# Kernel optimization log

Measured on AMD Instinct MI355X. Metric: run time of the kernel, lower is better.

## Reference

```python
import jax, jax.numpy as jnp
import numpy as np

N0, N1, N2, N3 = 1_000_000, 300_000, 80_000, 30_000
CIN, C = 4, 64  # in_channels, INIT_DIM / PLANES[0]
K = 27          # 3x3x3 octree kernel
EPS = 1e-5      # BatchNorm eps


def octree_conv(x, neigh, W):
    """Octree sparse conv as gather + GEMM.
    x: [Nin, Cin], neigh: [Nout, K] int indices into x, W: [K, Cin, Cout].
    """
    g = x[neigh]                              # [Nout, K, Cin] irregular gather
    return jnp.einsum('nkc,kcd->nd', g, W)    # [Nout, Cout]


def batchnorm(x, gamma, beta):
    # BatchNorm1d in training mode: batch stats over node dim, biased variance
    m = jnp.mean(x, axis=0)
    v = jnp.var(x, axis=0)
    return (x - m) * jax.lax.rsqrt(v + EPS) * gamma + beta


def setup_inputs() -> dict:
    key = jax.random.key(0)
    ks = jax.random.split(key, 16)
    s = 0.05
    return {
        'x': jax.random.normal(ks[0], (N0, CIN), jnp.float32),
        'neigh_stem': jax.random.randint(ks[1], (N1, K), 0, N0, jnp.int32),
        'pool_child': jax.random.randint(ks[2], (N2, 8), 0, N1, jnp.int32),
        'neigh_ds': jax.random.randint(ks[3], (N3, K), 0, N2, jnp.int32),
        'neigh_res': jax.random.randint(ks[4], (N3, K), 0, N3, jnp.int32),
        'W_stem': jax.random.normal(ks[5], (K, CIN, C), jnp.float32) * s,
        'g_stem': jnp.ones((C,), jnp.float32),
        'b_stem': jnp.zeros((C,), jnp.float32),
        'W1': jax.random.normal(ks[6], (K, C, C), jnp.float32) * s,
        'g1': jnp.ones((C,), jnp.float32),
        'b1': jnp.zeros((C,), jnp.float32),
        'W2': jax.random.normal(ks[7], (K, C, C), jnp.float32) * s,
        'g2': jnp.ones((C,), jnp.float32),
        'b2': jnp.zeros((C,), jnp.float32),
        'Wd': jax.random.normal(ks[8], (K, C, C), jnp.float32) * s,
        'gd': jnp.ones((C,), jnp.float32),
        'bd': jnp.zeros((C,), jnp.float32),
    }


def reference(x, neigh_stem, pool_child, neigh_ds, neigh_res,
              W_stem, g_stem, b_stem, W1, g1, b1, W2, g2, b2, Wd, gd, bd):
    # StemLayer: conv(s2) -> BN -> ReLU -> OctreeMaxPool
    h = jax.nn.relu(batchnorm(octree_conv(x, neigh_stem, W_stem), g_stem, b_stem))  # [N1, C]
    h = jnp.max(h[pool_child], axis=1)                                              # [N2, C]
    # ResBlock stride=2 (layer1, blocks=1)
    out = jax.nn.relu(batchnorm(octree_conv(h, neigh_ds, W1), g1, b1))              # [N3, C]
    out = batchnorm(octree_conv(out, neigh_res, W2), g2, b2)                        # [N3, C]
    residual = batchnorm(octree_conv(h, neigh_ds, Wd), gd, bd)                      # DownSample shortcut
    return jax.nn.relu(out + residual)
```

## Files before the change

kernel.cpp:

```cpp
#include <hip/hip_runtime.h>

constexpr int CN0 = 1000000;
constexpr int CN1 = 300000;
constexpr int CN2 = 80000;
constexpr int CN3 = 30000;
constexpr float BN_EPS = 1e-5f;

typedef __attribute__((ext_vector_type(8))) short bf16x8;
typedef __attribute__((ext_vector_type(4))) float f32x4;

union FragU { uint4 u; bf16x8 b; };

__device__ __forceinline__ float2 bn_ab(float s, float q, float invn, float gamma, float beta) {
  float m = s * invn;
  float v = fmaf(q, invn, -m * m);
  float rstd = rsqrtf(v + BN_EPS);
  float a = gamma * rstd;
  float b = beta - m * a;
  return make_float2(a, b);
}

__device__ __forceinline__ unsigned short f2bf(float f) {
  unsigned u = __float_as_uint(f);
  u += 0x7FFFu + ((u >> 16) & 1u);
  return (unsigned short)(u >> 16);
}

__device__ __forceinline__ void sync_lds() {
  asm volatile("s_waitcnt lgkmcnt(0)" ::: "memory");
  __builtin_amdgcn_s_barrier();
  asm volatile("" ::: "memory");
}

__global__ __launch_bounds__(256) void k_prep_x(
    const float* __restrict__ x, unsigned int* __restrict__ xbf) {
  int i = blockIdx.x * 256 + threadIdx.x;
  if (i >= CN0) return;
  float4 v = *(const float4*)(x + i * 4);
  uint2 p;
  p.x = (unsigned)f2bf(v.x) | ((unsigned)f2bf(v.y) << 16);
  p.y = (unsigned)f2bf(v.z) | ((unsigned)f2bf(v.w) << 16);
  *(uint2*)(xbf + i * 2) = p;
}

__global__ __launch_bounds__(256) void k_prep_stem(
    const float* __restrict__ W, unsigned short* __restrict__ Wf) {
  int f = blockIdx.x * 256 + threadIdx.x;
  if (f >= 8192) return;
  int e = f & 7, lane = (f >> 3) & 63, nf = (f >> 9) & 3, ks = f >> 11;
  int k = ks * 32 + (lane >> 4) * 8 + e;
  int d = nf * 16 + (lane & 15);
  Wf[f] = (k < 108) ? f2bf(W[k * 64 + d]) : (unsigned short)0;
}

__global__ __launch_bounds__(256) void k_prep_dual(
    const float* __restrict__ W1, const float* __restrict__ Wd,
    unsigned short* __restrict__ Wdual) {
  int e = blockIdx.x * 256 + threadIdx.x;
  if (e >= 27 * 128 * 64) return;
  int cin = e & 63, d = (e >> 6) & 127, k = e >> 13;
  float v = (d < 64) ? W1[(k * 64 + cin) * 64 + d]
                     : Wd[(k * 64 + cin) * 64 + (d - 64)];
  Wdual[e] = f2bf(v);
}

__global__ __launch_bounds__(256) void k_prep_res(
    const float* __restrict__ W2, unsigned short* __restrict__ Wres) {
  int e = blockIdx.x * 256 + threadIdx.x;
  if (e >= 27 * 64 * 64) return;
  int cin = e & 63, d = (e >> 6) & 63, k = e >> 12;
  Wres[e] = f2bf(W2[(k * 64 + cin) * 64 + d]);
}

__global__ __launch_bounds__(256) void k_stem_mfma(
    const unsigned short* __restrict__ xbf, const int* __restrict__ neigh,
    const unsigned short* __restrict__ Wf, unsigned short* __restrict__ y1,
    float* __restrict__ stats) {
  constexpr int T = 4;
  __shared__ __align__(16) uint4 Bb[1024];
  const int tid = threadIdx.x;
  const int lane = tid & 63;
  const int wv = tid >> 6;
  const int l15 = lane & 15, lq = lane >> 4;
  const int g0 = blockIdx.x * T;

  {
    const uint4* Wsrc = (const uint4*)Wf;
#pragma unroll
    for (int j = 0; j < 4; ++j) Bb[tid + j * 256] = Wsrc[tid + j * 256];
  }
  __syncthreads();

  int idxA[8], idxB[8];
  FragU fragA[4], fragB[4];

#define LDIDX(g, dst)                                                   \
  {                                                                     \
    int node_ = (g)*64 + wv * 16 + l15;                                 \
    bool rowok_ = node_ < CN1;                                          \
    const int* nb_ = neigh + node_ * 27;                                \
    _Pragma("unroll") for (int ks_ = 0; ks_ < 4; ++ks_) {               \
      int tap0_ = ks_ * 8 + lq * 2;                                     \
      dst[ks_ * 2] = (rowok_ && tap0_ < 27) ? nb_[tap0_] : -1;          \
      dst[ks_ * 2 + 1] = (rowok_ && tap0_ + 1 < 27) ? nb_[tap0_ + 1] : -1; \
    }                                                                   \
  }

#define GATHER(idx, frag)                                               \
  {                                                                     \
    _Pragma("unroll") for (int ks_ = 0; ks_ < 4; ++ks_) {               \
      uint2 v0_ = {0u, 0u}, v1_ = {0u, 0u};                             \
      if (idx[ks_ * 2] >= 0)                                            \
        v0_ = *(const uint2*)(xbf + idx[ks_ * 2] * 4);                  \
      if (idx[ks_ * 2 + 1] >= 0)                                        \
        v1_ = *(const uint2*)(xbf + idx[ks_ * 2 + 1] * 4);              \
      frag[ks_].u.x = v0_.x; frag[ks_].u.y = v0_.y;                     \
      frag[ks_].u.z = v1_.x; frag[ks_].u.w = v1_.y;                     \
    }                                                                   \
  }

  LDIDX(g0 + 0, idxA);
  GATHER(idxA, fragA);
  LDIDX(g0 + 1, idxB);

  float sacc[4] = {0.f, 0.f, 0.f, 0.f};
  float qacc[4] = {0.f, 0.f, 0.f, 0.f};

#pragma unroll
  for (int t = 0; t < T; ++t) {
    FragU* cur = (t & 1) ? fragB : fragA;
    FragU* nxt = (t & 1) ? fragA : fragB;
    int* idn = (t & 1) ? idxA : idxB;
    int* idn2 = (t & 1) ? idxB : idxA;
    if (t + 1 < T) GATHER(idn, nxt);
    if (t + 2 < T) LDIDX(g0 + t + 2, idn2);

    f32x4 acc[4] = {};
#pragma unroll
    for (int ks = 0; ks < 4; ++ks) {
#pragma unroll
      for (int nf = 0; nf < 4; ++nf) {
        bf16x8 b = *(const bf16x8*)&Bb[(ks * 4 + nf) * 64 + lane];
        acc[nf] = __builtin_amdgcn_mfma_f32_16x16x32_bf16(cur[ks].b, b,
                                                          acc[nf], 0, 0, 0);
      }
    }

    int n0 = (g0 + t) * 64 + wv * 16;
#pragma unroll
    for (int nf = 0; nf < 4; ++nf) {
      int c = nf * 16 + l15;
#pragma unroll
      for (int r = 0; r < 4; ++r) {
        int row = n0 + lq * 4 + r;
        float v = acc[nf][r];
        if (row < CN1) y1[row * 64 + c] = f2bf(v);
        sacc[nf] += v;
        qacc[nf] = fmaf(v, v, qacc[nf]);
      }
    }
  }
#undef LDIDX
#undef GATHER

  __syncthreads();
  float* S = (float*)Bb;
#pragma unroll
  for (int nf = 0; nf < 4; ++nf) {
    float s = sacc[nf], q = qacc[nf];
    s += __shfl_xor(s, 16); s += __shfl_xor(s, 32);
    q += __shfl_xor(q, 16); q += __shfl_xor(q, 32);
    if (lane < 16) {
      S[wv * 64 + nf * 16 + lane] = s;
      S[256 + wv * 64 + nf * 16 + lane] = q;
    }
  }
  __syncthreads();
  if (tid < 64) {
    float s = S[tid] + S[64 + tid] + S[128 + tid] + S[192 + tid];
    float q = S[256 + tid] + S[320 + tid] + S[384 + tid] + S[448 + tid];
    atomicAdd(&stats[tid], s);
    atomicAdd(&stats[64 + tid], q);
  }
}

__global__ __launch_bounds__(256) void k_pool(
    const unsigned int* __restrict__ y1, const int* __restrict__ child,
    const float* __restrict__ stats, const float* __restrict__ gamma,
    const float* __restrict__ beta, unsigned int* __restrict__ h2) {
  const int tid = threadIdx.x;
  const int wd = tid & 31;
  const int n = blockIdx.x * 8 + (tid >> 5);
  const int c0 = wd * 2, c1 = c0 + 1;
  const int* crow = child + n * 8;
  int ch[8];
#pragma unroll
  for (int j = 0; j < 8; ++j) ch[j] = crow[j];
  unsigned vv[8];
#pragma unroll
  for (int j = 0; j < 8; ++j) vv[j] = y1[ch[j] * 32 + wd];

  float2 ab0 = bn_ab(stats[c0], stats[64 + c0], 1.0f / CN1, gamma[c0], beta[c0]);
  float2 ab1 = bn_ab(stats[c1], stats[64 + c1], 1.0f / CN1, gamma[c1], beta[c1]);
  float mx0 = -INFINITY, mn0 = INFINITY, mx1 = -INFINITY, mn1 = INFINITY;
#pragma unroll
  for (int j = 0; j < 8; ++j) {
    float v0 = __uint_as_float(vv[j] << 16);
    float v1 = __uint_as_float(vv[j] & 0xFFFF0000u);
    mx0 = fmaxf(mx0, v0); mn0 = fminf(mn0, v0);
    mx1 = fmaxf(mx1, v1); mn1 = fminf(mn1, v1);
  }
  float t0 = (ab0.x > 0.f) ? fmaf(ab0.x, mx0, ab0.y) : fmaf(ab0.x, mn0, ab0.y);
  float t1 = (ab1.x > 0.f) ? fmaf(ab1.x, mx1, ab1.y) : fmaf(ab1.x, mn1, ab1.y);
  unsigned o = (unsigned)f2bf(fmaxf(t0, 0.f)) |
               ((unsigned)f2bf(fmaxf(t1, 0.f)) << 16);
  h2[n * 32 + wd] = o;
}

template <int OUTC>
__global__ __launch_bounds__(256) void k_mconv(
    const unsigned short* __restrict__ src, const int* __restrict__ neigh,
    const unsigned short* __restrict__ Wblk, float* __restrict__ out,
    float* __restrict__ stats, int M) {
  constexpr int NF = OUTC / 32;
  constexpr int PPT = (OUTC * 128 / 16) / 256;
  __shared__ __align__(16) unsigned char Ab[64 * 128];
  __shared__ __align__(16) unsigned char Bb[OUTC * 128];
  __shared__ int nlds[64 * 27];

  const int tid = threadIdx.x;
  const int n0 = blockIdx.x * 64;
  const int lane = tid & 63;
  const int w = tid >> 6;
  const int wm = w >> 1, wn = w & 1;
  const int gi = tid >> 2;
  const int gq = tid & 3;
  const int swA = (gi & 7) << 4;

  for (int e = tid; e < 64 * 27; e += 256) {
    int row = n0 + e / 27;
    nlds[e] = (row < M) ? neigh[row * 27 + e % 27] : -1;
  }

  f32x4 acc[2][NF] = {};
  uint4 rA0 = {}, rA1 = {};
  uint4 rB[PPT];

  sync_lds();

  {
    int idx = nlds[gi * 27 + 0];
    if (idx >= 0) {
      const uint4* s = (const uint4*)(src + idx * 64 + gq * 16);
      rA0 = s[0]; rA1 = s[1];
    } else {
      rA0 = uint4{0, 0, 0, 0}; rA1 = uint4{0, 0, 0, 0};
    }
    const uint4* Bs = (const uint4*)(Wblk);
#pragma unroll
    for (int j = 0; j < PPT; ++j) rB[j] = Bs[tid * PPT + j];
  }

  for (int k = 0; k < 27; ++k) {
    *(uint4*)(Ab + gi * 128 + ((gq * 32) ^ swA)) = rA0;
    *(uint4*)(Ab + gi * 128 + ((gq * 32 + 16) ^ swA)) = rA1;
#pragma unroll
    for (int j = 0; j < PPT; ++j) {
      int p = tid * PPT + j;
      int d = p >> 3;
      int rb = (p & 7) * 16;
      *(uint4*)(Bb + d * 128 + (rb ^ ((d & 7) << 4))) = rB[j];
    }
    if (k < 26) {
      int idx = nlds[gi * 27 + k + 1];
      if (idx >= 0) {
        const uint4* s = (const uint4*)(src + idx * 64 + gq * 16);
        rA0 = s[0]; rA1 = s[1];
      } else {
        rA0 = uint4{0, 0, 0, 0}; rA1 = uint4{0, 0, 0, 0};
      }
      const uint4* Bs = (const uint4*)(Wblk + (k + 1) * OUTC * 64);
#pragma unroll
      for (int j = 0; j < PPT; ++j) rB[j] = Bs[tid * PPT + j];
    }
    sync_lds();
#pragma unroll
    for (int ks = 0; ks < 2; ++ks) {
      int kb = ks * 64 + (lane >> 4) * 16;
      bf16x8 a[2];
#pragma unroll
      for (int mf = 0; mf < 2; ++mf) {
        int r = wm * 32 + mf * 16 + (lane & 15);
        a[mf] = *(const bf16x8*)(Ab + r * 128 + (kb ^ ((r & 7) << 4)));
      }
#pragma unroll
      for (int nf = 0; nf < NF; ++nf) {
        int d = wn * (OUTC / 2) + nf * 16 + (lane & 15);
        bf16x8 b = *(const bf16x8*)(Bb + d * 128 + (kb ^ ((d & 7) << 4)));
#pragma unroll
        for (int mf = 0; mf < 2; ++mf)
          acc[mf][nf] = __builtin_amdgcn_mfma_f32_16x16x32_bf16(
              a[mf], b, acc[mf][nf], 0, 0, 0);
      }
    }
    sync_lds();
  }

#pragma unroll
  for (int mf = 0; mf < 2; ++mf) {
    int rbase = n0 + wm * 32 + mf * 16 + (lane >> 4) * 4;
#pragma unroll
    for (int nf = 0; nf < NF; ++nf) {
      int c = wn * (OUTC / 2) + nf * 16 + (lane & 15);
#pragma unroll
      for (int r = 0; r < 4; ++r) {
        int row = rbase + r;
        if (row < M) out[row * OUTC + c] = acc[mf][nf][r];
      }
    }
  }

#pragma unroll
  for (int nf = 0; nf < NF; ++nf) {
    float s = 0.f, q = 0.f;
#pragma unroll
    for (int mf = 0; mf < 2; ++mf)
#pragma unroll
      for (int r = 0; r < 4; ++r) {
        float v = acc[mf][nf][r];
        s += v; q += v * v;
      }
    s += __shfl_xor(s, 16); s += __shfl_xor(s, 32);
    q += __shfl_xor(q, 16); q += __shfl_xor(q, 32);
    if (lane < 16) {
      int c = wn * (OUTC / 2) + nf * 16 + lane;
      atomicAdd(&stats[c], s);
      atomicAdd(&stats[OUTC + c], q);
    }
  }
}

__global__ __launch_bounds__(256) void k_bnrelu(
    const float* __restrict__ y2d, const float* __restrict__ stats,
    const float* __restrict__ gamma, const float* __restrict__ beta,
    unsigned short* __restrict__ out1) {
  int e = blockIdx.x * 256 + threadIdx.x;
  int i = e >> 6, c = e & 63;
  float2 ab = bn_ab(stats[c], stats[128 + c], 1.0f / CN3, gamma[c], beta[c]);
  out1[e] = f2bf(fmaxf(fmaf(ab.x, y2d[i * 128 + c], ab.y), 0.f));
}

__global__ __launch_bounds__(256) void k_final(
    const float* __restrict__ y3, const float* __restrict__ y2d,
    const float* __restrict__ stats2, const float* __restrict__ stats1d,
    const float* __restrict__ g2, const float* __restrict__ b2,
    const float* __restrict__ gd, const float* __restrict__ bd,
    float* __restrict__ dout) {
  int e = blockIdx.x * 256 + threadIdx.x;
  int i = e >> 6, c = e & 63;
  float2 ab2 = bn_ab(stats2[c], stats2[64 + c], 1.0f / CN3, g2[c], b2[c]);
  float2 abd =
      bn_ab(stats1d[64 + c], stats1d[192 + c], 1.0f / CN3, gd[c], bd[c]);
  float o = fmaf(ab2.x, y3[e], ab2.y) + fmaf(abd.x, y2d[i * 128 + 64 + c], abd.y);
  dout[e] = fmaxf(o, 0.f);
}

extern "C" void kernel_launch(void* const* d_in, const int* in_sizes, int n_in,
                              void* d_out, int out_size, void* d_ws,
                              size_t ws_size, hipStream_t stream) {
  const float* x = (const float*)d_in[0];
  const int* neigh_stem = (const int*)d_in[1];
  const int* pool_child = (const int*)d_in[2];
  const int* neigh_ds = (const int*)d_in[3];
  const int* neigh_res = (const int*)d_in[4];
  const float* W_stem = (const float*)d_in[5];
  const float* g_stem = (const float*)d_in[6];
  const float* b_stem = (const float*)d_in[7];
  const float* W1 = (const float*)d_in[8];
  const float* g1 = (const float*)d_in[9];
  const float* b1 = (const float*)d_in[10];
  const float* W2 = (const float*)d_in[11];
  const float* g2 = (const float*)d_in[12];
  const float* b2 = (const float*)d_in[13];
  const float* Wd = (const float*)d_in[14];
  const float* gd = (const float*)d_in[15];
  const float* bd = (const float*)d_in[16];
  float* out = (float*)d_out;
  float* ws = (float*)d_ws;

  unsigned short* y1bf = (unsigned short*)ws;
  float* y2d = ws;
  unsigned short* out1bf = (unsigned short*)(ws + 3840000);
  float* y3 = ws + 4800000;
  unsigned short* h2bf = (unsigned short*)(ws + 9600000);
  unsigned int* xbf = (unsigned int*)(ws + 12160000);
  unsigned short* Wst = (unsigned short*)(ws + 14160000);
  unsigned short* Wdual = (unsigned short*)(ws + 14164096);
  unsigned short* Wres = (unsigned short*)(ws + 14274688);
  float* stats = ws + 14329984;
  float* stats_stem = stats;
  float* stats_1d = stats + 128;
  float* stats_2 = stats + 384;

  hipMemsetAsync(stats, 0, 512 * sizeof(float), stream);

  k_prep_x<<<(CN0 + 255) / 256, 256, 0, stream>>>(x, xbf);
  k_prep_stem<<<(8192 + 255) / 256, 256, 0, stream>>>(W_stem, Wst);
  k_prep_dual<<<(27 * 128 * 64 + 255) / 256, 256, 0, stream>>>(W1, Wd, Wdual);
  k_prep_res<<<(27 * 64 * 64 + 255) / 256, 256, 0, stream>>>(W2, Wres);

  k_stem_mfma<<<1172, 256, 0, stream>>>(
      (const unsigned short*)xbf, neigh_stem, Wst, y1bf, stats_stem);
  k_pool<<<CN2 / 8, 256, 0, stream>>>((const unsigned int*)y1bf, pool_child,
                                      stats_stem, g_stem, b_stem,
                                      (unsigned int*)h2bf);
  k_mconv<128><<<(CN3 + 63) / 64, 256, 0, stream>>>(h2bf, neigh_ds, Wdual,
                                                    y2d, stats_1d, CN3);
  k_bnrelu<<<CN3 * 64 / 256, 256, 0, stream>>>(y2d, stats_1d, g1, b1, out1bf);
  k_mconv<64><<<(CN3 + 63) / 64, 256, 0, stream>>>(out1bf, neigh_res, Wres,
                                                   y3, stats_2, CN3);
  k_final<<<CN3 * 64 / 256, 256, 0, stream>>>(y3, y2d, stats_2, stats_1d, g2,
                                              b2, gd, bd, out);
}
```

Measured before the change: 277.5 us.

## Gather A fragments directly into registers and pre-swizzle weights for MFMA in conv kernels

The gather-conv kernel no longer stages gathered rows and weights through swizzled LDS tiles. Each lane now loads its MFMA A-fragment straight from global memory with a three-slot register pipeline. Weights are pre-permuted into MFMA fragment order and double-buffered in LDS with one barrier per tap, and blocks shrink to 32 nodes, so the grid gets larger. The stem kernel now handles 2 tiles per block instead of 4, issues both gathers up front, and overlaps the weight load with them. The cost is more register pressure, and weights are reloaded once per 32 nodes instead of once per 64.

After: 400.5 us. 1.44x slower.

```diff
diff --git a/kernel.cpp b/kernel.cpp
--- a/kernel.cpp
+++ b/kernel.cpp
@@ -44,97 +44,99 @@
 }
 
 __global__ __launch_bounds__(256) void k_prep_stem(
-    const float* __restrict__ W, unsigned short* __restrict__ Wf) {
+    const float* __restrict__ W, unsigned short* __restrict__ Wt) {
   int f = blockIdx.x * 256 + threadIdx.x;
   if (f >= 8192) return;
   int e = f & 7, lane = (f >> 3) & 63, nf = (f >> 9) & 3, ks = f >> 11;
   int k = ks * 32 + (lane >> 4) * 8 + e;
   int d = nf * 16 + (lane & 15);
-  Wf[f] = (k < 108) ? f2bf(W[k * 64 + d]) : (unsigned short)0;
+  Wt[f] = (k < 108) ? f2bf(W[k * 64 + d]) : (unsigned short)0;
 }
 
 __global__ __launch_bounds__(256) void k_prep_dual(
     const float* __restrict__ W1, const float* __restrict__ Wd,
-    unsigned short* __restrict__ Wdual) {
-  int e = blockIdx.x * 256 + threadIdx.x;
-  if (e >= 27 * 128 * 64) return;
-  int cin = e & 63, d = (e >> 6) & 127, k = e >> 13;
-  float v = (d < 64) ? W1[(k * 64 + cin) * 64 + d]
-                     : Wd[(k * 64 + cin) * 64 + (d - 64)];
-  Wdual[e] = f2bf(v);
+    unsigned short* __restrict__ Wf) {
+  int f = blockIdx.x * 256 + threadIdx.x;
+  if (f >= 27 * 8192) return;
+  int tap = f >> 13, r = f & 8191;
+  int ks1 = (r >> 12) & 1, nfg = (r >> 9) & 7, lane = (r >> 3) & 63, e = r & 7;
+  int cin = ks1 * 32 + (lane >> 4) * 8 + e;
+  int d = nfg * 16 + (lane & 15);
+  float v = (d < 64) ? W1[(tap * 64 + cin) * 64 + d]
+                     : Wd[(tap * 64 + cin) * 64 + (d - 64)];
+  Wf[f] = f2bf(v);
 }
 
 __global__ __launch_bounds__(256) void k_prep_res(
-    const float* __restrict__ W2, unsigned short* __restrict__ Wres) {
-  int e = blockIdx.x * 256 + threadIdx.x;
-  if (e >= 27 * 64 * 64) return;
-  int cin = e & 63, d = (e >> 6) & 63, k = e >> 12;
-  Wres[e] = f2bf(W2[(k * 64 + cin) * 64 + d]);
+    const float* __restrict__ W2, unsigned short* __restrict__ Wf) {
+  int f = blockIdx.x * 256 + threadIdx.x;
+  if (f >= 27 * 4096) return;
+  int tap = f >> 12, r = f & 4095;
+  int ks1 = (r >> 11) & 1, nfg = (r >> 9) & 3, lane = (r >> 3) & 63, e = r & 7;
+  int cin = ks1 * 32 + (lane >> 4) * 8 + e;
+  int d = nfg * 16 + (lane & 15);
+  Wf[f] = f2bf(W2[(tap * 64 + cin) * 64 + d]);
 }
 
 __global__ __launch_bounds__(256) void k_stem_mfma(
     const unsigned short* __restrict__ xbf, const int* __restrict__ neigh,
     const unsigned short* __restrict__ Wf, unsigned short* __restrict__ y1,
     float* __restrict__ stats) {
-  constexpr int T = 4;
   __shared__ __align__(16) uint4 Bb[1024];
   const int tid = threadIdx.x;
   const int lane = tid & 63;
   const int wv = tid >> 6;
   const int l15 = lane & 15, lq = lane >> 4;
-  const int g0 = blockIdx.x * T;
-
+  const int g0 = blockIdx.x * 2;
+
+  uint4 wreg[4];
   {
-    const uint4* Wsrc = (const uint4*)Wf;
-#pragma unroll
-    for (int j = 0; j < 4; ++j) Bb[tid + j * 256] = Wsrc[tid + j * 256];
-  }
-  __syncthreads();
-
-  int idxA[8], idxB[8];
-  FragU fragA[4], fragB[4];
-
-#define LDIDX(g, dst)                                                   \
-  {                                                                     \
-    int node_ = (g)*64 + wv * 16 + l15;                                 \
-    bool rowok_ = node_ < CN1;                                          \
-    const int* nb_ = neigh + node_ * 27;                                \
-    _Pragma("unroll") for (int ks_ = 0; ks_ < 4; ++ks_) {               \
-      int tap0_ = ks_ * 8 + lq * 2;                                     \
-      dst[ks_ * 2] = (rowok_ && tap0_ < 27) ? nb_[tap0_] : -1;          \
+    const uint4* Ws = (const uint4*)Wf;
+#pragma unroll
+    for (int j = 0; j < 4; ++j) wreg[j] = Ws[tid + j * 256];
+  }
+
+  int idx0[8], idx1[8];
+#define LDIDX(g, dst)                                                      \
+  {                                                                        \
+    int node_ = (g)*64 + wv * 16 + l15;                                    \
+    bool rowok_ = node_ < CN1;                                             \
+    const int* nb_ = neigh + node_ * 27;                                   \
+    _Pragma("unroll") for (int ks_ = 0; ks_ < 4; ++ks_) {                  \
+      int tap0_ = ks_ * 8 + lq * 2;                                        \
+      dst[ks_ * 2] = (rowok_ && tap0_ < 27) ? nb_[tap0_] : -1;             \
       dst[ks_ * 2 + 1] = (rowok_ && tap0_ + 1 < 27) ? nb_[tap0_ + 1] : -1; \
-    }                                                                   \
-  }
-
-#define GATHER(idx, frag)                                               \
-  {                                                                     \
-    _Pragma("unroll") for (int ks_ = 0; ks_ < 4; ++ks_) {               \
-      uint2 v0_ = {0u, 0u}, v1_ = {0u, 0u};                             \
-      if (idx[ks_ * 2] >= 0)                                            \
-        v0_ = *(const uint2*)(xbf + idx[ks_ * 2] * 4);                  \
-      if (idx[ks_ * 2 + 1] >= 0)                                        \
-        v1_ = *(const uint2*)(xbf + idx[ks_ * 2 + 1] * 4);              \
-      frag[ks_].u.x = v0_.x; frag[ks_].u.y = v0_.y;                     \
-      frag[ks_].u.z = v1_.x; frag[ks_].u.w = v1_.y;                     \
-    }                                                                   \
-  }
-
-  LDIDX(g0 + 0, idxA);
-  GATHER(idxA, fragA);
-  LDIDX(g0 + 1, idxB);
+    }                                                                      \
+  }
+#define GATHER(idx, frag)                                                  \
+  {                                                                        \
+    _Pragma("unroll") for (int ks_ = 0; ks_ < 4; ++ks_) {                  \
+      uint2 v0_ = {0u, 0u}, v1_ = {0u, 0u};                                \
+      if (idx[ks_ * 2] >= 0)                                               \
+        v0_ = *(const uint2*)(xbf + idx[ks_ * 2] * 4);                     \
+      if (idx[ks_ * 2 + 1] >= 0)                                           \
+        v1_ = *(const uint2*)(xbf + idx[ks_ * 2 + 1] * 4);                 \
+      frag[ks_].u.x = v0_.x; frag[ks_].u.y = v0_.y;                        \
+      frag[ks_].u.z = v1_.x; frag[ks_].u.w = v1_.y;                        \
+    }                                                                      \
+  }
+
+  LDIDX(g0 + 0, idx0);
+  LDIDX(g0 + 1, idx1);
+  FragU fA[4], fB[4];
+  GATHER(idx0, fA);
+  GATHER(idx1, fB);
+
+#pragma unroll
+  for (int j = 0; j < 4; ++j) Bb[tid + j * 256] = wreg[j];
+  sync_lds();
 
   float sacc[4] = {0.f, 0.f, 0.f, 0.f};
   float qacc[4] = {0.f, 0.f, 0.f, 0.f};
 
 #pragma unroll
-  for (int t = 0; t < T; ++t) {
-    FragU* cur = (t & 1) ? fragB : fragA;
-    FragU* nxt = (t & 1) ? fragA : fragB;
-    int* idn = (t & 1) ? idxA : idxB;
-    int* idn2 = (t & 1) ? idxB : idxA;
-    if (t + 1 < T) GATHER(idn, nxt);
-    if (t + 2 < T) LDIDX(g0 + t + 2, idn2);
-
+  for (int t = 0; t < 2; ++t) {
+    FragU* cur = t ? fB : fA;
     f32x4 acc[4] = {};
 #pragma unroll
     for (int ks = 0; ks < 4; ++ks) {
@@ -145,7 +147,6 @@
                                                           acc[nf], 0, 0, 0);
       }
     }
-
     int n0 = (g0 + t) * 64 + wv * 16;
 #pragma unroll
     for (int nf = 0; nf < 4; ++nf) {
@@ -163,7 +164,7 @@
 #undef LDIDX
 #undef GATHER
 
-  __syncthreads();
+  sync_lds();
   float* S = (float*)Bb;
 #pragma unroll
   for (int nf = 0; nf < 4; ++nf) {
@@ -218,122 +219,107 @@
 }
 
 template <int OUTC>
-__global__ __launch_bounds__(256) void k_mconv(
+__global__ __launch_bounds__(OUTC * 2) void k_mconv(
     const unsigned short* __restrict__ src, const int* __restrict__ neigh,
-    const unsigned short* __restrict__ Wblk, float* __restrict__ out,
+    const unsigned short* __restrict__ Wf, float* __restrict__ out,
     float* __restrict__ stats, int M) {
-  constexpr int NF = OUTC / 32;
-  constexpr int PPT = (OUTC * 128 / 16) / 256;
-  __shared__ __align__(16) unsigned char Ab[64 * 128];
-  __shared__ __align__(16) unsigned char Bb[OUTC * 128];
-  __shared__ int nlds[64 * 27];
+  constexpr int CG = OUTC / 64;
+  constexpr int THREADS = OUTC * 2;
+  constexpr int PT = CG * 512;
+  __shared__ __align__(16) uint4 Bb[2][PT];
 
   const int tid = threadIdx.x;
-  const int n0 = blockIdx.x * 64;
   const int lane = tid & 63;
   const int w = tid >> 6;
-  const int wm = w >> 1, wn = w & 1;
-  const int gi = tid >> 2;
-  const int gq = tid & 3;
-  const int swA = (gi & 7) << 4;
-
-  for (int e = tid; e < 64 * 27; e += 256) {
-    int row = n0 + e / 27;
-    nlds[e] = (row < M) ? neigh[row * 27 + e % 27] : -1;
-  }
-
-  f32x4 acc[2][NF] = {};
-  uint4 rA0 = {}, rA1 = {};
-  uint4 rB[PPT];
-
+  const int ng = w & 1, cg = w >> 1;
+  const int l15 = lane & 15, lq = lane >> 4;
+  const int node = blockIdx.x * 32 + ng * 16 + l15;
+  const bool ok = node < M;
+  const int* nb = neigh + node * 27;
+  const uint4* WfU = (const uint4*)Wf;
+
+  uint4 rB[2][4];
+#pragma unroll
+  for (int j = 0; j < 4; ++j) rB[0][j] = WfU[j * THREADS + tid];
+#pragma unroll
+  for (int j = 0; j < 4; ++j) rB[1][j] = WfU[PT + j * THREADS + tid];
+
+  int ixv[4];
+#pragma unroll
+  for (int t = 0; t < 4; ++t) ixv[t] = ok ? nb[t] : -1;
+
+  FragU aA[3][2];
+#define MGATHER(slot, ixval)                                        \
+  {                                                                 \
+    int ix_ = (ixval);                                              \
+    if (ix_ >= 0) {                                                 \
+      const char* bp_ = (const char*)src + (size_t)ix_ * 128 + lq * 16; \
+      aA[slot][0].u = *(const uint4*)(bp_);                         \
+      aA[slot][1].u = *(const uint4*)(bp_ + 64);                    \
+    } else {                                                        \
+      aA[slot][0].u = uint4{0u, 0u, 0u, 0u};                        \
+      aA[slot][1].u = uint4{0u, 0u, 0u, 0u};                        \
+    }                                                               \
+  }
+  MGATHER(0, ixv[0]);
+  MGATHER(1, ixv[1]);
+
+#pragma unroll
+  for (int j = 0; j < 4; ++j) Bb[0][j * THREADS + tid] = rB[0][j];
   sync_lds();
 
-  {
-    int idx = nlds[gi * 27 + 0];
-    if (idx >= 0) {
-      const uint4* s = (const uint4*)(src + idx * 64 + gq * 16);
-      rA0 = s[0]; rA1 = s[1];
-    } else {
-      rA0 = uint4{0, 0, 0, 0}; rA1 = uint4{0, 0, 0, 0};
-    }
-    const uint4* Bs = (const uint4*)(Wblk);
-#pragma unroll
-    for (int j = 0; j < PPT; ++j) rB[j] = Bs[tid * PPT + j];
-  }
-
+  f32x4 acc[4] = {};
+#pragma unroll
   for (int k = 0; k < 27; ++k) {
-    *(uint4*)(Ab + gi * 128 + ((gq * 32) ^ swA)) = rA0;
-    *(uint4*)(Ab + gi * 128 + ((gq * 32 + 16) ^ swA)) = rA1;
-#pragma unroll
-    for (int j = 0; j < PPT; ++j) {
-      int p = tid * PPT + j;
-      int d = p >> 3;
-      int rb = (p & 7) * 16;
-      *(uint4*)(Bb + d * 128 + (rb ^ ((d & 7) << 4))) = rB[j];
-    }
-    if (k < 26) {
-      int idx = nlds[gi * 27 + k + 1];
-      if (idx >= 0) {
-        const uint4* s = (const uint4*)(src + idx * 64 + gq * 16);
-        rA0 = s[0]; rA1 = s[1];
-      } else {
-        rA0 = uint4{0, 0, 0, 0}; rA1 = uint4{0, 0, 0, 0};
-      }
-      const uint4* Bs = (const uint4*)(Wblk + (k + 1) * OUTC * 64);
-#pragma unroll
-      for (int j = 0; j < PPT; ++j) rB[j] = Bs[tid * PPT + j];
-    }
-    sync_lds();
-#pragma unroll
-    for (int ks = 0; ks < 2; ++ks) {
-      int kb = ks * 64 + (lane >> 4) * 16;
-      bf16x8 a[2];
-#pragma unroll
-      for (int mf = 0; mf < 2; ++mf) {
-        int r = wm * 32 + mf * 16 + (lane & 15);
-        a[mf] = *(const bf16x8*)(Ab + r * 128 + (kb ^ ((r & 7) << 4)));
-      }
-#pragma unroll
-      for (int nf = 0; nf < NF; ++nf) {
-        int d = wn * (OUTC / 2) + nf * 16 + (lane & 15);
-        bf16x8 b = *(const bf16x8*)(Bb + d * 128 + (kb ^ ((d & 7) << 4)));
-#pragma unroll
-        for (int mf = 0; mf < 2; ++mf)
-          acc[mf][nf] = __builtin_amdgcn_mfma_f32_16x16x32_bf16(
-              a[mf], b, acc[mf][nf], 0, 0, 0);
-      }
-    }
-    sync_lds();
-  }
-
-#pragma unroll
-  for (int mf = 0; mf < 2; ++mf) {
-    int rbase = n0 + wm * 32 + mf * 16 + (lane >> 4) * 4;
-#pragma unroll
-    for (int nf = 0; nf < NF; ++nf) {
-      int c = wn * (OUTC / 2) + nf * 16 + (lane & 15);
-#pragma unroll
-      for (int r = 0; r < 4; ++r) {
-        int row = rbase + r;
-        if (row < M) out[row * OUTC + c] = acc[mf][nf][r];
-      }
-    }
-  }
-
-#pragma unroll
-  for (int nf = 0; nf < NF; ++nf) {
+    if (k + 2 < 27) {
+#pragma unroll
+      for (int j = 0; j < 4; ++j)
+        rB[k & 1][j] = WfU[(k + 2) * PT + j * THREADS + tid];
+      MGATHER((k + 2) % 3, ixv[(k + 2) % 4]);
+    }
+    if (k + 4 < 27) ixv[(k + 4) % 4] = ok ? nb[k + 4] : -1;
+#pragma unroll
+    for (int nf = 0; nf < 4; ++nf) {
+      bf16x8 b0 = *(const bf16x8*)&Bb[k & 1][(cg * 4 + nf) * 64 + lane];
+      acc[nf] = __builtin_amdgcn_mfma_f32_16x16x32_bf16(aA[k % 3][0].b, b0,
+                                                        acc[nf], 0, 0, 0);
+      bf16x8 b1 =
+          *(const bf16x8*)&Bb[k & 1][(CG * 4 + cg * 4 + nf) * 64 + lane];
+      acc[nf] = __builtin_amdgcn_mfma_f32_16x16x32_bf16(aA[k % 3][1].b, b1,
+                                                        acc[nf], 0, 0, 0);
+    }
+    if (k + 1 < 27) {
+#pragma unroll
+      for (int j = 0; j < 4; ++j)
+        Bb[(k + 1) & 1][j * THREADS + tid] = rB[(k + 1) & 1][j];
+      sync_lds();
+    }
+  }
+#undef MGATHER
+
+  const int rowbase = blockIdx.x * 32 + ng * 16 + lq * 4;
+#pragma unroll
+  for (int nf = 0; nf < 4; ++nf) {
+    int c = cg * 64 + nf * 16 + l15;
+#pragma unroll
+    for (int r = 0; r < 4; ++r) {
+      int row = rowbase + r;
+      if (row < M) out[row * OUTC + c] = acc[nf][r];
+    }
+  }
+
+#pragma unroll
+  for (int nf = 0; nf < 4; ++nf) {
     float s = 0.f, q = 0.f;
 #pragma unroll
-    for (int mf = 0; mf < 2; ++mf)
-#pragma unroll
-      for (int r = 0; r < 4; ++r) {
-        float v = acc[mf][nf][r];
-        s += v; q += v * v;
-      }
+    for (int r = 0; r < 4; ++r) {
+      float v = acc[nf][r];
+      s += v; q += v * v;
+    }
     s += __shfl_xor(s, 16); s += __shfl_xor(s, 32);
     q += __shfl_xor(q, 16); q += __shfl_xor(q, 32);
     if (lane < 16) {
-      int c = wn * (OUTC / 2) + nf * 16 + lane;
+      int c = cg * 64 + nf * 16 + lane;
       atomicAdd(&stats[c], s);
       atomicAdd(&stats[OUTC + c], q);
     }
@@ -406,18 +392,18 @@
 
   k_prep_x<<<(CN0 + 255) / 256, 256, 0, stream>>>(x, xbf);
   k_prep_stem<<<(8192 + 255) / 256, 256, 0, stream>>>(W_stem, Wst);
-  k_prep_dual<<<(27 * 128 * 64 + 255) / 256, 256, 0, stream>>>(W1, Wd, Wdual);
-  k_prep_res<<<(27 * 64 * 64 + 255) / 256, 256, 0, stream>>>(W2, Wres);
-
-  k_stem_mfma<<<1172, 256, 0, stream>>>(
+  k_prep_dual<<<(27 * 8192 + 255) / 256, 256, 0, stream>>>(W1, Wd, Wdual);
+  k_prep_res<<<(27 * 4096 + 255) / 256, 256, 0, stream>>>(W2, Wres);
+
+  k_stem_mfma<<<2344, 256, 0, stream>>>(
       (const unsigned short*)xbf, neigh_stem, Wst, y1bf, stats_stem);
   k_pool<<<CN2 / 8, 256, 0, stream>>>((const unsigned int*)y1bf, pool_child,
                                       stats_stem, g_stem, b_stem,
                                       (unsigned int*)h2bf);
-  k_mconv<128><<<(CN3 + 63) / 64, 256, 0, stream>>>(h2bf, neigh_ds, Wdual,
+  k_mconv<128><<<(CN3 + 31) / 32, 256, 0, stream>>>(h2bf, neigh_ds, Wdual,
                                                     y2d, stats_1d, CN3);
   k_bnrelu<<<CN3 * 64 / 256, 256, 0, stream>>>(y2d, stats_1d, g1, b1, out1bf);
-  k_mconv<64><<<(CN3 + 63) / 64, 256, 0, stream>>>(out1bf, neigh_res, Wres,
+  k_mconv<64><<<(CN3 + 31) / 32, 128, 0, stream>>>(out1bf, neigh_res, Wres,
                                                    y3, stats_2, CN3);
   k_final<<<CN3 * 64 / 256, 256, 0, stream>>>(y3, y2d, stats_2, stats_1d, g2,
                                               b2, gd, bd, out);
```
